# Kernel tuning notes

Measured on AMD Instinct MI355X. Metric: run time of the kernel, lower is better.

Reference implementation:

```python
import jax, jax.numpy as jnp
import numpy as np

N_NODES = 100000
N_EDGES = 1600000
D_NODE = 96
D_EDGE = 32
N_GRAPHS = 128
BN_EPS = 1e-5


def setup_inputs() -> dict:
    key = jax.random.key(0)
    ks = jax.random.split(key, 8)
    x = jax.random.normal(ks[0], (N_NODES, D_NODE), dtype=jnp.float32)
    edge_attr = jax.random.normal(ks[1], (N_EDGES, D_EDGE), dtype=jnp.float32)
    edge_index = jax.random.randint(ks[2], (2, N_EDGES), 0, N_NODES, dtype=jnp.int64)
    batch = jnp.sort(jax.random.randint(ks[3], (N_NODES,), 0, N_GRAPHS, dtype=jnp.int64))
    W1 = jax.random.normal(ks[4], (16, D_NODE + D_EDGE), dtype=jnp.float32) * 0.09
    b1 = jax.random.normal(ks[5], (16,), dtype=jnp.float32) * 0.01
    gamma = jnp.ones((16,), dtype=jnp.float32)
    beta = jnp.zeros((16,), dtype=jnp.float32)
    run_mean = jnp.zeros((16,), dtype=jnp.float32)
    run_var = jnp.ones((16,), dtype=jnp.float32)
    W2 = jax.random.normal(ks[6], (1, 16), dtype=jnp.float32) * 0.25
    b2 = jax.random.normal(ks[7], (1,), dtype=jnp.float32) * 0.01
    return {"x": x, "edge_attr": edge_attr, "edge_index": edge_index, "batch": batch,
            "W1": W1, "b1": b1, "gamma": gamma, "beta": beta,
            "run_mean": run_mean, "run_var": run_var, "W2": W2, "b2": b2}


def reference(x, edge_attr, edge_index, batch, W1, b1, gamma, beta, run_mean, run_var, W2, b2):
    src, dst = edge_index[0], edge_index[1]
    # per-edge message: MLP(cat([x_j, edge_attr]))  -- [E, d_node+d_edge]
    msg_in = jnp.concatenate([x[src], edge_attr], axis=1)
    h = msg_in @ W1.T + b1                                  # [E, 16]
    # BatchNorm1d in eval mode (running stats); Dropout is identity in eval
    h = gamma * (h - run_mean) * jax.lax.rsqrt(run_var + BN_EPS) + beta
    h = jax.nn.relu(h)
    msg = h @ W2.T + b2                                     # [E, 1]
    # scatter-add messages to target nodes
    node_out = jax.ops.segment_sum(msg, dst, num_segments=N_NODES)   # [N, 1]
    # global add pool per graph
    pooled = jax.ops.segment_sum(node_out, batch, num_segments=N_GRAPHS)  # [G, 1]
    # mean over feature dim (size 1)
    return jnp.mean(pooled, axis=1)                         # [G]
```

## Files before the change

kernel.cpp:

```cpp
#include <hip/hip_runtime.h>

#define N_NODES 100000
#define N_EDGES 1600000
#define D_NODE 96
#define D_EDGE 32
#define N_GRAPHS 128
#define BN_EPS 1e-5f

#define EDGE_BLOCKS 2048
#define EDGE_THREADS 256

__global__ void prep_kernel(const float* __restrict__ W1, const float* __restrict__ b1,
                            const float* __restrict__ gamma, const float* __restrict__ beta,
                            const float* __restrict__ rmean, const float* __restrict__ rvar,
                            const float* __restrict__ W2, const float* __restrict__ b2,
                            float* __restrict__ w1n, float* __restrict__ w1e,
                            float* __restrict__ cw) {
    int t = threadIdx.x;
    if (t < 16) {
        float A = gamma[t] * rsqrtf(rvar[t] + BN_EPS);
        cw[t] = A * (b1[t] - rmean[t]) + beta[t];
        cw[16 + t] = W2[t];
        for (int j = 0; j < D_NODE; ++j)
            w1n[t * D_NODE + j] = A * W1[t * (D_NODE + D_EDGE) + j];
        for (int j = 0; j < D_EDGE; ++j)
            w1e[t * D_EDGE + j] = A * W1[t * (D_NODE + D_EDGE) + D_NODE + j];
    }
    if (t == 16) cw[32] = b2[0];
}

__global__ __launch_bounds__(256) void node_proj_kernel(const float* __restrict__ x,
                                                        const float* __restrict__ w1n,
                                                        float* __restrict__ y) {
    int n = blockIdx.x * 256 + threadIdx.x;
    if (n >= N_NODES) return;
    const float4* xr = (const float4*)(x + (size_t)n * D_NODE);
    float acc[16];
#pragma unroll
    for (int k = 0; k < 16; ++k) acc[k] = 0.f;
#pragma unroll
    for (int j4 = 0; j4 < D_NODE / 4; ++j4) {
        float4 xv = xr[j4];
#pragma unroll
        for (int k = 0; k < 16; ++k) {
            const float* w = w1n + k * D_NODE + j4 * 4;
            acc[k] += xv.x * w[0] + xv.y * w[1] + xv.z * w[2] + xv.w * w[3];
        }
    }
    float4* yr = (float4*)(y + (size_t)n * 16);
#pragma unroll
    for (int q = 0; q < 4; ++q)
        yr[q] = make_float4(acc[q * 4 + 0], acc[q * 4 + 1], acc[q * 4 + 2], acc[q * 4 + 3]);
}

__global__ __launch_bounds__(EDGE_THREADS) void edge_kernel(
    const float* __restrict__ ea, const int* __restrict__ eidx,
    const int* __restrict__ batch, const float* __restrict__ y,
    const float* __restrict__ w1e, const float* __restrict__ cw,
    float* __restrict__ partials) {
    __shared__ float bins[N_GRAPHS];
    int t = threadIdx.x;
    if (t < N_GRAPHS) bins[t] = 0.f;
    __syncthreads();

    const int* srcp = eidx;
    const int* dstp = eidx + N_EDGES;
    float b2v = cw[32];

    for (int e = blockIdx.x * EDGE_THREADS + t; e < N_EDGES; e += EDGE_BLOCKS * EDGE_THREADS) {
        int s = srcp[e];
        int d = dstp[e];

        const float4* er = (const float4*)(ea + (size_t)e * D_EDGE);
        float4 ev[8];
#pragma unroll
        for (int i = 0; i < 8; ++i) ev[i] = er[i];

        float ya[16];
        const float4* yr = (const float4*)(y + (size_t)s * 16);
#pragma unroll
        for (int q = 0; q < 4; ++q) ((float4*)ya)[q] = yr[q];

        float msg = b2v;
#pragma unroll
        for (int k = 0; k < 16; ++k) {
            float z = 0.f;
#pragma unroll
            for (int i = 0; i < 8; ++i) {
                const float* w = w1e + k * D_EDGE + i * 4;
                z += ev[i].x * w[0] + ev[i].y * w[1] + ev[i].z * w[2] + ev[i].w * w[3];
            }
            float h = z + ya[k] + cw[k];
            msg += fmaxf(h, 0.f) * cw[16 + k];
        }

        int g = batch[d];
        atomicAdd(&bins[g], msg);
    }

    __syncthreads();
    if (t < N_GRAPHS) partials[(size_t)blockIdx.x * N_GRAPHS + t] = bins[t];
}

__global__ __launch_bounds__(256) void reduce_kernel(const float* __restrict__ partials,
                                                     float* __restrict__ out) {
    __shared__ float s[256];
    int g = blockIdx.x;
    float acc = 0.f;
    for (int b = threadIdx.x; b < EDGE_BLOCKS; b += 256)
        acc += partials[(size_t)b * N_GRAPHS + g];
    s[threadIdx.x] = acc;
    __syncthreads();
    for (int w = 128; w > 0; w >>= 1) {
        if (threadIdx.x < w) s[threadIdx.x] += s[threadIdx.x + w];
        __syncthreads();
    }
    if (threadIdx.x == 0) out[g] = s[0];
}

extern "C" void kernel_launch(void* const* d_in, const int* in_sizes, int n_in,
                              void* d_out, int out_size, void* d_ws, size_t ws_size,
                              hipStream_t stream) {
    const float* x     = (const float*)d_in[0];
    const float* ea    = (const float*)d_in[1];
    const int*   eidx  = (const int*)d_in[2];
    const int*   batch = (const int*)d_in[3];
    const float* W1    = (const float*)d_in[4];
    const float* b1    = (const float*)d_in[5];
    const float* gamma = (const float*)d_in[6];
    const float* beta  = (const float*)d_in[7];
    const float* rmean = (const float*)d_in[8];
    const float* rvar  = (const float*)d_in[9];
    const float* W2    = (const float*)d_in[10];
    const float* b2    = (const float*)d_in[11];
    float* out = (float*)d_out;

    float* ws = (float*)d_ws;
    float* w1n      = ws;
    float* w1e      = ws + 1536;
    float* cw       = ws + 2048;
    float* y        = ws + 4096;
    float* partials = ws + 4096 + (size_t)N_NODES * 16;

    prep_kernel<<<1, 64, 0, stream>>>(W1, b1, gamma, beta, rmean, rvar, W2, b2, w1n, w1e, cw);
    node_proj_kernel<<<(N_NODES + 255) / 256, 256, 0, stream>>>(x, w1n, y);
    edge_kernel<<<EDGE_BLOCKS, EDGE_THREADS, 0, stream>>>(ea, eidx, batch, y, w1e, cw, partials);
    reduce_kernel<<<N_GRAPHS, 256, 0, stream>>>(partials, out);
}
```

Baseline: 395.1 us.

## Split node projection across threads and use one edge per thread with transposed partials

The node projection now assigns four threads per node, each computing four of the sixteen outputs, which raises thread count and lowers per-thread register use. The edge kernel drops the grid-stride loop in favour of one edge per thread over many more blocks. It streams the edge features one float4 at a time into sixteen accumulators instead of holding all eight vectors, and adds an occupancy hint to launch_bounds. Partial sums are written in a transposed, padded layout so the reduction reads contiguously, at the cost of more blocks and more partials to reduce.

```diff
diff --git a/kernel.cpp b/kernel.cpp
--- a/kernel.cpp
+++ b/kernel.cpp
@@ -7,8 +7,9 @@
 #define N_GRAPHS 128
 #define BN_EPS 1e-5f
 
-#define EDGE_BLOCKS 2048
+#define EDGE_BLOCKS 6250
 #define EDGE_THREADS 256
+#define PT_STRIDE 6272
 
 __global__ void prep_kernel(const float* __restrict__ W1, const float* __restrict__ b1,
                             const float* __restrict__ gamma, const float* __restrict__ beta,
@@ -32,90 +33,89 @@
 __global__ __launch_bounds__(256) void node_proj_kernel(const float* __restrict__ x,
                                                         const float* __restrict__ w1n,
                                                         float* __restrict__ y) {
-    int n = blockIdx.x * 256 + threadIdx.x;
+    int t = threadIdx.x;
+    int q = t >> 6;
+    int n = blockIdx.x * 64 + (t & 63);
     if (n >= N_NODES) return;
     const float4* xr = (const float4*)(x + (size_t)n * D_NODE);
-    float acc[16];
+    const float* wq = w1n + (q * 4) * D_NODE;
+    float acc[4];
 #pragma unroll
-    for (int k = 0; k < 16; ++k) acc[k] = 0.f;
+    for (int kk = 0; kk < 4; ++kk) acc[kk] = 0.f;
 #pragma unroll
     for (int j4 = 0; j4 < D_NODE / 4; ++j4) {
         float4 xv = xr[j4];
 #pragma unroll
-        for (int k = 0; k < 16; ++k) {
-            const float* w = w1n + k * D_NODE + j4 * 4;
-            acc[k] += xv.x * w[0] + xv.y * w[1] + xv.z * w[2] + xv.w * w[3];
+        for (int kk = 0; kk < 4; ++kk) {
+            const float* w = wq + kk * D_NODE + j4 * 4;
+            acc[kk] += xv.x * w[0] + xv.y * w[1] + xv.z * w[2] + xv.w * w[3];
         }
     }
-    float4* yr = (float4*)(y + (size_t)n * 16);
-#pragma unroll
-    for (int q = 0; q < 4; ++q)
-        yr[q] = make_float4(acc[q * 4 + 0], acc[q * 4 + 1], acc[q * 4 + 2], acc[q * 4 + 3]);
+    ((float4*)(y + (size_t)n * 16))[q] = make_float4(acc[0], acc[1], acc[2], acc[3]);
 }
 
-__global__ __launch_bounds__(EDGE_THREADS) void edge_kernel(
+__global__ __launch_bounds__(EDGE_THREADS, 8) void edge_kernel(
     const float* __restrict__ ea, const int* __restrict__ eidx,
     const int* __restrict__ batch, const float* __restrict__ y,
     const float* __restrict__ w1e, const float* __restrict__ cw,
-    float* __restrict__ partials) {
+    float* __restrict__ partialsT) {
     __shared__ float bins[N_GRAPHS];
     int t = threadIdx.x;
     if (t < N_GRAPHS) bins[t] = 0.f;
     __syncthreads();
 
-    const int* srcp = eidx;
-    const int* dstp = eidx + N_EDGES;
-    float b2v = cw[32];
-
-    for (int e = blockIdx.x * EDGE_THREADS + t; e < N_EDGES; e += EDGE_BLOCKS * EDGE_THREADS) {
-        int s = srcp[e];
-        int d = dstp[e];
-
-        const float4* er = (const float4*)(ea + (size_t)e * D_EDGE);
-        float4 ev[8];
-#pragma unroll
-        for (int i = 0; i < 8; ++i) ev[i] = er[i];
+    int e = blockIdx.x * EDGE_THREADS + t;
+    if (e < N_EDGES) {
+        int s = eidx[e];
+        int d = eidx[N_EDGES + e];
+        int g = batch[d];
 
         float ya[16];
         const float4* yr = (const float4*)(y + (size_t)s * 16);
 #pragma unroll
-        for (int q = 0; q < 4; ++q) ((float4*)ya)[q] = yr[q];
+        for (int qq = 0; qq < 4; ++qq) ((float4*)ya)[qq] = yr[qq];
 
-        float msg = b2v;
+        const float4* er = (const float4*)(ea + (size_t)e * D_EDGE);
+        float acc[16];
+#pragma unroll
+        for (int k = 0; k < 16; ++k) acc[k] = 0.f;
+#pragma unroll 2
+        for (int i = 0; i < 8; ++i) {
+            float4 ev = er[i];
+#pragma unroll
+            for (int k = 0; k < 16; ++k) {
+                const float* w = w1e + k * D_EDGE + i * 4;
+                acc[k] += ev.x * w[0] + ev.y * w[1] + ev.z * w[2] + ev.w * w[3];
+            }
+        }
+
+        float msg = cw[32];
 #pragma unroll
         for (int k = 0; k < 16; ++k) {
-            float z = 0.f;
-#pragma unroll
-            for (int i = 0; i < 8; ++i) {
-                const float* w = w1e + k * D_EDGE + i * 4;
-                z += ev[i].x * w[0] + ev[i].y * w[1] + ev[i].z * w[2] + ev[i].w * w[3];
-            }
-            float h = z + ya[k] + cw[k];
+            float h = acc[k] + ya[k] + cw[k];
             msg += fmaxf(h, 0.f) * cw[16 + k];
         }
-
-        int g = batch[d];
         atomicAdd(&bins[g], msg);
     }
 
     __syncthreads();
-    if (t < N_GRAPHS) partials[(size_t)blockIdx.x * N_GRAPHS + t] = bins[t];
+    if (t < N_GRAPHS) partialsT[(size_t)t * PT_STRIDE + blockIdx.x] = bins[t];
 }
 
-__global__ __launch_bounds__(256) void reduce_kernel(const float* __restrict__ partials,
+__global__ __launch_bounds__(256) void reduce_kernel(const float* __restrict__ partialsT,
                                                      float* __restrict__ out) {
-    __shared__ float s[256];
+    __shared__ float sm[256];
     int g = blockIdx.x;
     float acc = 0.f;
     for (int b = threadIdx.x; b < EDGE_BLOCKS; b += 256)
-        acc += partials[(size_t)b * N_GRAPHS + g];
-    s[threadIdx.x] = acc;
+        acc += partialsT[(size_t)g * PT_STRIDE + b];
+    sm[threadIdx.x] = acc;
     __syncthreads();
     for (int w = 128; w > 0; w >>= 1) {
-        if (threadIdx.x < w) s[threadIdx.x] += s[threadIdx.x + w];
+        if (threadIdx.x < w) sm[threadIdx.x] += sm[threadIdx.x + w];
         __syncthreads();
     }
-    if (threadIdx.x == 0) out[g] = s[0];
+    if (threadIdx.x == 0) out[g] = sm[0];
 }
 
 extern "C" void kernel_launch(void* const* d_in, const int* in_sizes, int n_in,
@@ -136,14 +136,14 @@
     float* out = (float*)d_out;
 
     float* ws = (float*)d_ws;
-    float* w1n      = ws;
-    float* w1e      = ws + 1536;
-    float* cw       = ws + 2048;
-    float* y        = ws + 4096;
-    float* partials = ws + 4096 + (size_t)N_NODES * 16;
+    float* w1n       = ws;
+    float* w1e       = ws + 1536;
+    float* cw        = ws + 2048;
+    float* y         = ws + 4096;
+    float* partialsT = ws + 4096 + (size_t)N_NODES * 16;
 
     prep_kernel<<<1, 64, 0, stream>>>(W1, b1, gamma, beta, rmean, rvar, W2, b2, w1n, w1e, cw);
-    node_proj_kernel<<<(N_NODES + 255) / 256, 256, 0, stream>>>(x, w1n, y);
-    edge_kernel<<<EDGE_BLOCKS, EDGE_THREADS, 0, stream>>>(ea, eidx, batch, y, w1e, cw, partials);
-    reduce_kernel<<<N_GRAPHS, 256, 0, stream>>>(partials, out);
+    node_proj_kernel<<<(N_NODES + 63) / 64, 256, 0, stream>>>(x, w1n, y);
+    edge_kernel<<<EDGE_BLOCKS, EDGE_THREADS, 0, stream>>>(ea, eidx, batch, y, w1e, cw, partialsT);
+    reduce_kernel<<<N_GRAPHS, 256, 0, stream>>>(partialsT, out);
 }
```

New measurement: 434.1 us. +9.9%, slower.

## Transpose weights, use packed f2 FMAs, one edge per thread grid

Applied to the files above, without the earlier changes.

Weights are stored transposed so each input element broadcasts against contiguous output columns, and the inner products use packed two-wide FMA builtins. The node projection splits the 16 outputs across four threads per node for more parallelism. The edge kernel drops its grid-stride loop and launches one thread per edge (6250 blocks, occupancy hint 8), which makes the partials buffer and the reduce larger. The kernel remains bound on memory traffic from edge_attr and the gathers, so the packed math may matter less than the change in occupancy and access pattern.

```diff
diff --git a/kernel.cpp b/kernel.cpp
--- a/kernel.cpp
+++ b/kernel.cpp
@@ -7,14 +7,16 @@
 #define N_GRAPHS 128
 #define BN_EPS 1e-5f
 
-#define EDGE_BLOCKS 2048
+#define EDGE_BLOCKS 6250
 #define EDGE_THREADS 256
+
+typedef float f2 __attribute__((ext_vector_type(2)));
 
 __global__ void prep_kernel(const float* __restrict__ W1, const float* __restrict__ b1,
                             const float* __restrict__ gamma, const float* __restrict__ beta,
                             const float* __restrict__ rmean, const float* __restrict__ rvar,
                             const float* __restrict__ W2, const float* __restrict__ b2,
-                            float* __restrict__ w1n, float* __restrict__ w1e,
+                            float* __restrict__ w1nT, float* __restrict__ w1eT,
                             float* __restrict__ cw) {
     int t = threadIdx.x;
     if (t < 16) {
@@ -22,81 +24,91 @@
         cw[t] = A * (b1[t] - rmean[t]) + beta[t];
         cw[16 + t] = W2[t];
         for (int j = 0; j < D_NODE; ++j)
-            w1n[t * D_NODE + j] = A * W1[t * (D_NODE + D_EDGE) + j];
+            w1nT[j * 16 + t] = A * W1[t * (D_NODE + D_EDGE) + j];
         for (int j = 0; j < D_EDGE; ++j)
-            w1e[t * D_EDGE + j] = A * W1[t * (D_NODE + D_EDGE) + D_NODE + j];
+            w1eT[j * 16 + t] = A * W1[t * (D_NODE + D_EDGE) + D_NODE + j];
     }
     if (t == 16) cw[32] = b2[0];
 }
 
 __global__ __launch_bounds__(256) void node_proj_kernel(const float* __restrict__ x,
-                                                        const float* __restrict__ w1n,
+                                                        const float* __restrict__ w1nT,
                                                         float* __restrict__ y) {
-    int n = blockIdx.x * 256 + threadIdx.x;
+    int t = threadIdx.x;
+    int q = t >> 6;
+    int n = blockIdx.x * 64 + (t & 63);
     if (n >= N_NODES) return;
     const float4* xr = (const float4*)(x + (size_t)n * D_NODE);
-    float acc[16];
-#pragma unroll
-    for (int k = 0; k < 16; ++k) acc[k] = 0.f;
+    f2 acc0 = {0.f, 0.f}, acc1 = {0.f, 0.f};
 #pragma unroll
     for (int j4 = 0; j4 < D_NODE / 4; ++j4) {
         float4 xv = xr[j4];
 #pragma unroll
-        for (int k = 0; k < 16; ++k) {
-            const float* w = w1n + k * D_NODE + j4 * 4;
-            acc[k] += xv.x * w[0] + xv.y * w[1] + xv.z * w[2] + xv.w * w[3];
+        for (int u = 0; u < 4; ++u) {
+            float xs = (u == 0) ? xv.x : (u == 1) ? xv.y : (u == 2) ? xv.z : xv.w;
+            f2 xs2 = {xs, xs};
+            const f2* wp = (const f2*)(w1nT + (j4 * 4 + u) * 16 + q * 4);
+            acc0 = __builtin_elementwise_fma(xs2, wp[0], acc0);
+            acc1 = __builtin_elementwise_fma(xs2, wp[1], acc1);
         }
     }
-    float4* yr = (float4*)(y + (size_t)n * 16);
-#pragma unroll
-    for (int q = 0; q < 4; ++q)
-        yr[q] = make_float4(acc[q * 4 + 0], acc[q * 4 + 1], acc[q * 4 + 2], acc[q * 4 + 3]);
+    ((float4*)(y + (size_t)n * 16))[q] = make_float4(acc0.x, acc0.y, acc1.x, acc1.y);
 }
 
-__global__ __launch_bounds__(EDGE_THREADS) void edge_kernel(
+__global__ __launch_bounds__(EDGE_THREADS, 8) void edge_kernel(
     const float* __restrict__ ea, const int* __restrict__ eidx,
     const int* __restrict__ batch, const float* __restrict__ y,
-    const float* __restrict__ w1e, const float* __restrict__ cw,
+    const float* __restrict__ w1eT, const float* __restrict__ cw,
     float* __restrict__ partials) {
     __shared__ float bins[N_GRAPHS];
     int t = threadIdx.x;
     if (t < N_GRAPHS) bins[t] = 0.f;
     __syncthreads();
 
-    const int* srcp = eidx;
-    const int* dstp = eidx + N_EDGES;
-    float b2v = cw[32];
+    int e = blockIdx.x * EDGE_THREADS + t;
 
-    for (int e = blockIdx.x * EDGE_THREADS + t; e < N_EDGES; e += EDGE_BLOCKS * EDGE_THREADS) {
-        int s = srcp[e];
-        int d = dstp[e];
+    int sn = eidx[e];
+    int dn = eidx[N_EDGES + e];
+    int g  = batch[dn];
 
-        const float4* er = (const float4*)(ea + (size_t)e * D_EDGE);
-        float4 ev[8];
+    float ya[16];
+    const float4* yr = (const float4*)(y + (size_t)sn * 16);
 #pragma unroll
-        for (int i = 0; i < 8; ++i) ev[i] = er[i];
+    for (int qq = 0; qq < 4; ++qq) ((float4*)ya)[qq] = yr[qq];
 
-        float ya[16];
-        const float4* yr = (const float4*)(y + (size_t)s * 16);
+    const float4* er = (const float4*)(ea + (size_t)e * D_EDGE);
+    float4 ev[8];
 #pragma unroll
-        for (int q = 0; q < 4; ++q) ((float4*)ya)[q] = yr[q];
+    for (int i = 0; i < 8; ++i) ev[i] = er[i];
 
-        float msg = b2v;
+    f2 acc[8];
 #pragma unroll
-        for (int k = 0; k < 16; ++k) {
-            float z = 0.f;
+    for (int k2 = 0; k2 < 8; ++k2) acc[k2] = (f2){0.f, 0.f};
+
+    const float* evs = (const float*)ev;
 #pragma unroll
-            for (int i = 0; i < 8; ++i) {
-                const float* w = w1e + k * D_EDGE + i * 4;
-                z += ev[i].x * w[0] + ev[i].y * w[1] + ev[i].z * w[2] + ev[i].w * w[3];
-            }
-            float h = z + ya[k] + cw[k];
-            msg += fmaxf(h, 0.f) * cw[16 + k];
-        }
+    for (int j = 0; j < D_EDGE; ++j) {
+        float b = evs[j];
+        f2 b2 = {b, b};
+        const f2* wp = (const f2*)(w1eT + j * 16);
+#pragma unroll
+        for (int k2 = 0; k2 < 8; ++k2)
+            acc[k2] = __builtin_elementwise_fma(b2, wp[k2], acc[k2]);
+    }
 
-        int g = batch[d];
-        atomicAdd(&bins[g], msg);
+    const f2* ya2 = (const f2*)ya;
+    const f2* c2  = (const f2*)cw;
+    const f2* w2p = (const f2*)(cw + 16);
+    f2 m2 = {0.f, 0.f};
+#pragma unroll
+    for (int k2 = 0; k2 < 8; ++k2) {
+        f2 h = acc[k2] + ya2[k2] + c2[k2];
+        h = __builtin_elementwise_max(h, (f2){0.f, 0.f});
+        m2 = __builtin_elementwise_fma(h, w2p[k2], m2);
     }
+    float msg = m2.x + m2.y + cw[32];
+
+    atomicAdd(&bins[g], msg);
 
     __syncthreads();
     if (t < N_GRAPHS) partials[(size_t)blockIdx.x * N_GRAPHS + t] = bins[t];
@@ -104,18 +116,18 @@
 
 __global__ __launch_bounds__(256) void reduce_kernel(const float* __restrict__ partials,
                                                      float* __restrict__ out) {
-    __shared__ float s[256];
+    __shared__ float sm[256];
     int g = blockIdx.x;
     float acc = 0.f;
     for (int b = threadIdx.x; b < EDGE_BLOCKS; b += 256)
         acc += partials[(size_t)b * N_GRAPHS + g];
-    s[threadIdx.x] = acc;
+    sm[threadIdx.x] = acc;
     __syncthreads();
     for (int w = 128; w > 0; w >>= 1) {
-        if (threadIdx.x < w) s[threadIdx.x] += s[threadIdx.x + w];
+        if (threadIdx.x < w) sm[threadIdx.x] += sm[threadIdx.x + w];
         __syncthreads();
     }
-    if (threadIdx.x == 0) out[g] = s[0];
+    if (threadIdx.x == 0) out[g] = sm[0];
 }
 
 extern "C" void kernel_launch(void* const* d_in, const int* in_sizes, int n_in,
@@ -136,14 +148,14 @@
     float* out = (float*)d_out;
 
     float* ws = (float*)d_ws;
-    float* w1n      = ws;
-    float* w1e      = ws + 1536;
+    float* w1nT     = ws;
+    float* w1eT     = ws + 1536;
     float* cw       = ws + 2048;
     float* y        = ws + 4096;
     float* partials = ws + 4096 + (size_t)N_NODES * 16;
 
-    prep_kernel<<<1, 64, 0, stream>>>(W1, b1, gamma, beta, rmean, rvar, W2, b2, w1n, w1e, cw);
-    node_proj_kernel<<<(N_NODES + 255) / 256, 256, 0, stream>>>(x, w1n, y);
-    edge_kernel<<<EDGE_BLOCKS, EDGE_THREADS, 0, stream>>>(ea, eidx, batch, y, w1e, cw, partials);
+    prep_kernel<<<1, 64, 0, stream>>>(W1, b1, gamma, beta, rmean, rvar, W2, b2, w1nT, w1eT, cw);
+    node_proj_kernel<<<(N_NODES + 63) / 64, 256, 0, stream>>>(x, w1nT, y);
+    edge_kernel<<<EDGE_BLOCKS, EDGE_THREADS, 0, stream>>>(ea, eidx, batch, y, w1eT, cw, partials);
     reduce_kernel<<<N_GRAPHS, 256, 0, stream>>>(partials, out);
 }
```

Result: slower. 413.8 us (+4.7%).
